# Performance work log

Measured on AMD Instinct MI355X. Metric: run time of the kernel, lower is better.

The kernel has to match this reference:

```python
import jax, jax.numpy as jnp
import numpy as np

BLUR = 0.05
P = 2
EPS_FINAL = BLUR ** P          # geomloss: eps = blur**p = 0.0025
DIAMETER = 2.0                 # max cosine cost magnitude
SCALING = 0.5                  # geomloss default; eps decays by scaling**p per step
N_FINAL_ITERS = 4              # extra balancing iterations at the final eps


def eps_schedule():
    eps_list = []
    e = DIAMETER ** P
    while e > EPS_FINAL:
        eps_list.append(e)
        e = e * (SCALING ** P)
    eps_list.extend([EPS_FINAL] * N_FINAL_ITERS)
    return eps_list


def cosine_cost(a, b):
    # a: (N, D), b: (M, D) -> (N, M) cost = 1 - cos_sim
    an = a / (jnp.linalg.norm(a, axis=1, keepdims=True) + 1e-12)
    bn = b / (jnp.linalg.norm(b, axis=1, keepdims=True) + 1e-12)
    return 1.0 - an @ bn.T


def softmin(C, pot, log_w, eps):
    # -eps * LSE_j( log_w + (pot_j - C_ij)/eps ) ; C: (N, M), pot: (M,)
    return -eps * jax.nn.logsumexp(log_w + (pot[None, :] - C) / eps, axis=1)


def sinkhorn_divergence(Cxy, Cxx, Cyy):
    N, M = Cxy.shape
    log_a = -jnp.log(jnp.asarray(N, dtype=Cxy.dtype))  # uniform weights
    log_b = -jnp.log(jnp.asarray(M, dtype=Cxy.dtype))
    sg = jax.lax.stop_gradient
    # Sinkhorn iterations run on detached costs (geomloss envelope-theorem trick)
    Cxy_s, Cxx_s, Cyy_s = sg(Cxy), sg(Cxx), sg(Cyy)
    f = jnp.zeros((N,), Cxy.dtype)
    g = jnp.zeros((M,), Cxy.dtype)
    fxx = jnp.zeros((N,), Cxy.dtype)
    gyy = jnp.zeros((M,), Cxy.dtype)
    for eps in eps_schedule():
        # symmetric (debiasing) potentials: averaged fixed-point update
        fxx = 0.5 * (fxx + softmin(Cxx_s, fxx, log_a, eps))
        gyy = 0.5 * (gyy + softmin(Cyy_s, gyy, log_b, eps))
        # cross potentials: simultaneous (Jacobi) update
        f, g = softmin(Cxy_s, g, log_b, eps), softmin(Cxy_s.T, f, log_a, eps)
    # final extrapolation step with gradients flowing through the costs
    eps = EPS_FINAL
    f_fin = softmin(Cxy, sg(g), log_b, eps)
    g_fin = softmin(Cxy.T, sg(f), log_a, eps)
    fxx_fin = softmin(Cxx, sg(fxx), log_a, eps)
    gyy_fin = softmin(Cyy, sg(gyy), log_b, eps)
    return jnp.mean(f_fin - fxx_fin) + jnp.mean(g_fin - gyy_fin)


def setup_inputs() -> dict:
    key = jax.random.key(0)
    k1, k2, k3 = jax.random.split(key, 3)
    x1 = jax.random.normal(k1, (8192, 256), dtype=jnp.float32)
    x2 = jax.random.normal(k2, (8192, 256), dtype=jnp.float32)
    w = jax.random.uniform(k3, (256,), dtype=jnp.float32)
    return {"x1": x1, "x2": x2, "w": w}


def reference(x1, x2, w):
    # Dist_loss.forward: clamp+renormalize learned per-feature weights, scale x1
    w_c = jnp.clip(w, 0.0, 2.0)
    w_c = w_c / jnp.mean(w_c)
    a = w_c[None, :] * x1
    Cxy = cosine_cost(a, x2)
    Cxx = cosine_cost(a, a)
    Cyy = cosine_cost(x2, x2)
    return sinkhorn_divergence(Cxy, Cxx, Cyy)
```

## Files before the change

kernel.cpp:

```cpp
#include <hip/hip_runtime.h>
#include <math.h>

#define N 8192
#define D 256
#define LN2 0.6931471805599453f
#define LDSROW 280
#define TSLOTS 1152

typedef short short8 __attribute__((ext_vector_type(8)));
typedef float f32x16 __attribute__((ext_vector_type(16)));
typedef unsigned short ushort;

__device__ __forceinline__ float fexp2(float x) { return __builtin_amdgcn_exp2f(x); }
__device__ __forceinline__ float flog2(float x) { return __builtin_amdgcn_logf(x); }

__device__ __forceinline__ ushort bf16r(float x) {
    unsigned int u = __float_as_uint(x);
    return (ushort)((u + 0x7FFF + ((u >> 16) & 1)) >> 16);
}

__device__ __forceinline__ void gl_lds16(const ushort* g, ushort* l) {
    __builtin_amdgcn_global_load_lds(
        (const __attribute__((address_space(1))) unsigned int*)g,
        (__attribute__((address_space(3))) unsigned int*)l, 16, 0, 0);
}

__global__ void prep_wc(const float* __restrict__ w, float* __restrict__ wc) {
    int t = threadIdx.x;
    float v = fminf(fmaxf(w[t], 0.0f), 2.0f);
    float s = v;
#pragma unroll
    for (int m = 1; m < 64; m <<= 1) s += __shfl_xor(s, m);
    __shared__ float sm[4];
    if ((t & 63) == 0) sm[t >> 6] = s;
    __syncthreads();
    float mean = (sm[0] + sm[1] + sm[2] + sm[3]) * (1.0f / 256.0f);
    wc[t] = v / mean;
}

__global__ void prep_normalize(const float* __restrict__ x1, const float* __restrict__ x2,
                               const float* __restrict__ wc,
                               ushort* __restrict__ an_i, ushort* __restrict__ bn_i) {
    int row = blockIdx.x;
    int t = threadIdx.x;
    int r; float v; ushort* ip;
    if (row < N) { r = row;     v = x1[(size_t)r * D + t] * wc[t]; ip = an_i; }
    else         { r = row - N; v = x2[(size_t)r * D + t];         ip = bn_i; }
    float ss = v * v;
#pragma unroll
    for (int m = 1; m < 64; m <<= 1) ss += __shfl_xor(ss, m);
    __shared__ float sm[4];
    if ((t & 63) == 0) sm[t >> 6] = ss;
    __syncthreads();
    float denom = sqrtf(sm[0] + sm[1] + sm[2] + sm[3]) + 1e-12f;
    ip[(size_t)r * D + t] = bf16r(v / denom);
}

__global__ void init_pots(float* __restrict__ pots, float* __restrict__ potm1) {
    int id = blockIdx.x * 256 + threadIdx.x;
    pots[id] = 0.0f;
    potm1[id] = -1.0f;
}

__global__ __launch_bounds__(256, 2) void softmin_mfma(
    const ushort* __restrict__ an_i, const ushort* __restrict__ bn_i,
    const float* __restrict__ potm1,
    float2* __restrict__ parts, float k1) {
    int bx = blockIdx.x;
    int k = bx & 7;
    int q = bx >> 3;
    int task = k >> 1;
    int split = ((k & 1) << 1) | (q & 1);
    int rb = q >> 1;
    const ushort* jp = (task == 0 || task == 3) ? an_i : bn_i;
    const ushort* ip = (task == 0 || task == 2) ? an_i : bn_i;
    const float* pm1 = potm1 + (size_t)task * N;

    int t = threadIdx.x;
    int wave = t >> 6, lane = t & 63;
    int l31 = lane & 31, lh = lane >> 5;
    int i0 = rb * 256 + wave * 64;

    __shared__ ushort lbuf[2][TSLOTS * 8];

    short8 bi0[16], bi1[16];
    {
        const ushort* ib = ip + (size_t)(i0 + l31) * D + lh * 8;
#pragma unroll
        for (int c = 0; c < 16; ++c) {
            bi0[c] = *(const short8*)(ib + c * 16);
            bi1[c] = *(const short8*)(ib + (size_t)32 * D + c * 16);
        }
    }
#pragma unroll
    for (int c = 0; c < 16; ++c) {
        asm volatile("" : "+a"(bi0[c]), "+a"(bi1[c]));
    }

    const int jbase0 = split * 2048;

    auto stage = [&](int b, int js) {
        const ushort* gb = jp + (size_t)(jbase0 + js * 32) * D;
        ushort* lb = &lbuf[b][0];
#pragma unroll
        for (int r = 0; r < 5; ++r) {
            if (r == 4 && t >= 128) break;
            int s = r * 256 + t;
            int row = s / 35;
            int c = s - row * 35;
            row = row > 31 ? 31 : row;
            c = c > 31 ? 31 : c;
            gl_lds16(gb + row * D + c * 8, lb + s * 8);
        }
    };

    float m0 = -INFINITY, s0 = 0.0f, m1 = -INFINITY, s1 = 0.0f;

    stage(0, 0);
    for (int js = 0; js < 64; ++js) {
        int cur = js & 1;
        __syncthreads();

        int j0 = jbase0 + js * 32;
        float pjk[16];
#pragma unroll
        for (int g = 0; g < 4; ++g) {
            float4 pv = *(const float4*)&pm1[j0 + 8 * g + 4 * lh];
            pjk[4 * g + 0] = pv.x * k1; pjk[4 * g + 1] = pv.y * k1;
            pjk[4 * g + 2] = pv.z * k1; pjk[4 * g + 3] = pv.w * k1;
        }

        if (js < 63) stage(cur ^ 1, js + 1);

        const ushort* lrow = &lbuf[cur][l31 * LDSROW + lh * 8];
        f32x16 acc0 = {}; f32x16 acc1 = {};
#pragma unroll
        for (int c = 0; c < 16; ++c) {
            short8 af = *(const short8*)(lrow + c * 16);
            acc0 = __builtin_amdgcn_mfma_f32_32x32x16_bf16(af, bi0[c], acc0, 0, 0, 0);
            acc1 = __builtin_amdgcn_mfma_f32_32x32x16_bf16(af, bi1[c], acc1, 0, 0, 0);
        }

        {
            float tv[16];
#pragma unroll
            for (int r = 0; r < 16; ++r) tv[r] = fmaf(acc0[r], k1, pjk[r]);
            float tm = tv[0];
#pragma unroll
            for (int r = 1; r < 16; ++r) tm = fmaxf(tm, tv[r]);
            float mn = fmaxf(m0, tm);
            float ad = 0.0f;
#pragma unroll
            for (int r = 0; r < 16; ++r) ad += fexp2(tv[r] - mn);
            s0 = s0 * fexp2(m0 - mn) + ad; m0 = mn;
        }
        {
            float tv[16];
#pragma unroll
            for (int r = 0; r < 16; ++r) tv[r] = fmaf(acc1[r], k1, pjk[r]);
            float tm = tv[0];
#pragma unroll
            for (int r = 1; r < 16; ++r) tm = fmaxf(tm, tv[r]);
            float mn = fmaxf(m1, tm);
            float ad = 0.0f;
#pragma unroll
            for (int r = 0; r < 16; ++r) ad += fexp2(tv[r] - mn);
            s1 = s1 * fexp2(m1 - mn) + ad; m1 = mn;
        }
    }
    float mo = __shfl_xor(m0, 32), so = __shfl_xor(s0, 32);
    float M0 = fmaxf(m0, mo);
    float S0 = s0 * fexp2(m0 - M0) + so * fexp2(mo - M0);
    mo = __shfl_xor(m1, 32); so = __shfl_xor(s1, 32);
    float M1 = fmaxf(m1, mo);
    float S1 = s1 * fexp2(m1 - M1) + so * fexp2(mo - M1);
    if (lane < 32) {
        size_t r0 = (size_t)task * N + (i0 + l31);
        size_t r1 = r0 + 32;
        parts[r0 * 4 + split] = make_float2(M0, S0);
        parts[r1 * 4 + split] = make_float2(M1, S1);
    }
}

__global__ void merge_pots(const float2* __restrict__ parts, float* __restrict__ pots,
                           float* __restrict__ potm1, float eps, float logw, int do_avg) {
    int id = blockIdx.x * 256 + threadIdx.x;
    int task = id >> 13;
    int row = id & (N - 1);
    const float2* p = parts + (size_t)id * 4;
    float2 a = p[0], b = p[1], c = p[2], d = p[3];
    float M = fmaxf(fmaxf(a.x, b.x), fmaxf(c.x, d.x));
    float S = a.y * fexp2(a.x - M) + b.y * fexp2(b.x - M) +
              c.y * fexp2(c.x - M) + d.y * fexp2(d.x - M);
    float lse = LN2 * (M + flog2(S));
    float v = -eps * (logw + lse);
    if (do_avg && task < 2) v = 0.5f * (pots[id] + v);
    pots[id] = v;
    int ct = (task < 2) ? task : (5 - task);
    potm1[(size_t)ct * N + row] = v - 1.0f;
}

__global__ void final_reduce(const float* __restrict__ pots, float* __restrict__ out) {
    int t = threadIdx.x;
    float s = 0.0f;
    for (int i = t; i < N; i += 256)
        s += (pots[2 * N + i] - pots[i]) + (pots[3 * N + i] - pots[N + i]);
#pragma unroll
    for (int m = 1; m < 64; m <<= 1) s += __shfl_xor(s, m);
    __shared__ float sm[4];
    if ((t & 63) == 0) sm[t >> 6] = s;
    __syncthreads();
    if (t == 0) out[0] = (sm[0] + sm[1] + sm[2] + sm[3]) * (1.0f / (float)N);
}

extern "C" void kernel_launch(void* const* d_in, const int* in_sizes, int n_in,
                              void* d_out, int out_size, void* d_ws, size_t ws_size,
                              hipStream_t stream) {
    const float* x1 = (const float*)d_in[0];
    const float* x2 = (const float*)d_in[1];
    const float* w  = (const float*)d_in[2];
    float* out = (float*)d_out;

    ushort* an_i = (ushort*)d_ws;
    ushort* bn_i = an_i + (size_t)N * D;
    float*  wc   = (float*)(bn_i + (size_t)N * D);
    float*  pots = wc + 256;
    float*  potm1 = pots + 4 * N;
    float2* parts = (float2*)(potm1 + 4 * N);

    prep_wc<<<1, 256, 0, stream>>>(w, wc);
    prep_normalize<<<2 * N, 256, 0, stream>>>(x1, x2, wc, an_i, bn_i);
    init_pots<<<4 * N / 256, 256, 0, stream>>>(pots, potm1);

    const float eps_list[10] = {4.0f, 1.0f, 0.25f, 0.0625f, 0.015625f,
                                0.00390625f, 0.0025f, 0.0025f, 0.0025f, 0.0025f};
    const float logw = -logf((float)N);
    const float LOG2E = 1.4426950408889634f;
    for (int it = 0; it < 10; ++it) {
        softmin_mfma<<<512, 256, 0, stream>>>(an_i, bn_i, potm1, parts, LOG2E / eps_list[it]);
        merge_pots<<<4 * N / 256, 256, 0, stream>>>(parts, pots, potm1,
                                                    eps_list[it], logw, 1);
    }
    softmin_mfma<<<512, 256, 0, stream>>>(an_i, bn_i, potm1, parts, LOG2E / 0.0025f);
    merge_pots<<<4 * N / 256, 256, 0, stream>>>(parts, pots, potm1, 0.0025f, logw, 0);
    final_reduce<<<1, 256, 0, stream>>>(pots, out);
}
```

Baseline: 1.813 ms.

## Repartition softmin into 768 blocks with 32 rows per wave and 3-way column split

Each wave now owns one 32-row tile instead of two, and the column range is split three ways (86/86/84 tiles) instead of four, so the grid becomes 768 blocks at three blocks per CU. The merge kernel combines three partial logsumexp pairs per row. The aim is a more even spread of work across CUs and higher occupancy through fewer registers per thread. The cost is that each LDS-staged column tile now feeds only one MFMA chain per wave instead of two, halving reuse of the shared tile and raising LDS and global traffic per FLOP.

```diff
diff --git a/kernel.cpp b/kernel.cpp
--- a/kernel.cpp
+++ b/kernel.cpp
@@ -62,16 +62,15 @@
     potm1[id] = -1.0f;
 }
 
-__global__ __launch_bounds__(256, 2) void softmin_mfma(
+__global__ __launch_bounds__(256, 3) void softmin_mfma(
     const ushort* __restrict__ an_i, const ushort* __restrict__ bn_i,
     const float* __restrict__ potm1,
     float2* __restrict__ parts, float k1) {
     int bx = blockIdx.x;
-    int k = bx & 7;
-    int q = bx >> 3;
-    int task = k >> 1;
-    int split = ((k & 1) << 1) | (q & 1);
-    int rb = q >> 1;
+    int c = bx % 12;
+    int rb = bx / 12;
+    int task = c & 3;
+    int split = c >> 2;
     const ushort* jp = (task == 0 || task == 3) ? an_i : bn_i;
     const ushort* ip = (task == 0 || task == 2) ? an_i : bn_i;
     const float* pm1 = potm1 + (size_t)task * N;
@@ -79,49 +78,48 @@
     int t = threadIdx.x;
     int wave = t >> 6, lane = t & 63;
     int l31 = lane & 31, lh = lane >> 5;
-    int i0 = rb * 256 + wave * 64;
+    int i0 = rb * 128 + wave * 32;
 
     __shared__ ushort lbuf[2][TSLOTS * 8];
 
-    short8 bi0[16], bi1[16];
+    short8 bi[16];
     {
         const ushort* ib = ip + (size_t)(i0 + l31) * D + lh * 8;
 #pragma unroll
-        for (int c = 0; c < 16; ++c) {
-            bi0[c] = *(const short8*)(ib + c * 16);
-            bi1[c] = *(const short8*)(ib + (size_t)32 * D + c * 16);
-        }
-    }
-#pragma unroll
-    for (int c = 0; c < 16; ++c) {
-        asm volatile("" : "+a"(bi0[c]), "+a"(bi1[c]));
-    }
-
-    const int jbase0 = split * 2048;
+        for (int cc = 0; cc < 16; ++cc) bi[cc] = *(const short8*)(ib + cc * 16);
+    }
+#pragma unroll
+    for (int cc = 0; cc < 16; ++cc) {
+        asm volatile("" : "+a"(bi[cc]));
+    }
+
+    int jb = split * 86;
+    int je = (split == 2) ? 256 : jb + 86;
 
     auto stage = [&](int b, int js) {
-        const ushort* gb = jp + (size_t)(jbase0 + js * 32) * D;
+        const ushort* gb = jp + (size_t)js * 32 * D;
         ushort* lb = &lbuf[b][0];
 #pragma unroll
         for (int r = 0; r < 5; ++r) {
             if (r == 4 && t >= 128) break;
             int s = r * 256 + t;
             int row = s / 35;
-            int c = s - row * 35;
+            int cs = s - row * 35;
             row = row > 31 ? 31 : row;
-            c = c > 31 ? 31 : c;
-            gl_lds16(gb + row * D + c * 8, lb + s * 8);
+            cs = cs > 31 ? 31 : cs;
+            gl_lds16(gb + row * D + cs * 8, lb + s * 8);
         }
     };
 
-    float m0 = -INFINITY, s0 = 0.0f, m1 = -INFINITY, s1 = 0.0f;
-
-    stage(0, 0);
-    for (int js = 0; js < 64; ++js) {
+    float m0 = -INFINITY, s0 = 0.0f;
+
+    stage(0, jb);
+    for (int js = jb; js < je; ++js) {
         int cur = js & 1;
         __syncthreads();
-
-        int j0 = jbase0 + js * 32;
+        if (js + 1 < je) stage(cur ^ 1, js + 1);
+
+        int j0 = js * 32;
         float pjk[16];
 #pragma unroll
         for (int g = 0; g < 4; ++g) {
@@ -130,55 +128,32 @@
             pjk[4 * g + 2] = pv.z * k1; pjk[4 * g + 3] = pv.w * k1;
         }
 
-        if (js < 63) stage(cur ^ 1, js + 1);
-
         const ushort* lrow = &lbuf[cur][l31 * LDSROW + lh * 8];
-        f32x16 acc0 = {}; f32x16 acc1 = {};
-#pragma unroll
-        for (int c = 0; c < 16; ++c) {
-            short8 af = *(const short8*)(lrow + c * 16);
-            acc0 = __builtin_amdgcn_mfma_f32_32x32x16_bf16(af, bi0[c], acc0, 0, 0, 0);
-            acc1 = __builtin_amdgcn_mfma_f32_32x32x16_bf16(af, bi1[c], acc1, 0, 0, 0);
+        f32x16 acc = {};
+#pragma unroll
+        for (int cc = 0; cc < 16; ++cc) {
+            short8 af = *(const short8*)(lrow + cc * 16);
+            acc = __builtin_amdgcn_mfma_f32_32x32x16_bf16(af, bi[cc], acc, 0, 0, 0);
         }
 
-        {
-            float tv[16];
-#pragma unroll
-            for (int r = 0; r < 16; ++r) tv[r] = fmaf(acc0[r], k1, pjk[r]);
-            float tm = tv[0];
-#pragma unroll
-            for (int r = 1; r < 16; ++r) tm = fmaxf(tm, tv[r]);
-            float mn = fmaxf(m0, tm);
-            float ad = 0.0f;
-#pragma unroll
-            for (int r = 0; r < 16; ++r) ad += fexp2(tv[r] - mn);
-            s0 = s0 * fexp2(m0 - mn) + ad; m0 = mn;
-        }
-        {
-            float tv[16];
-#pragma unroll
-            for (int r = 0; r < 16; ++r) tv[r] = fmaf(acc1[r], k1, pjk[r]);
-            float tm = tv[0];
-#pragma unroll
-            for (int r = 1; r < 16; ++r) tm = fmaxf(tm, tv[r]);
-            float mn = fmaxf(m1, tm);
-            float ad = 0.0f;
-#pragma unroll
-            for (int r = 0; r < 16; ++r) ad += fexp2(tv[r] - mn);
-            s1 = s1 * fexp2(m1 - mn) + ad; m1 = mn;
-        }
+        float tv[16];
+#pragma unroll
+        for (int r = 0; r < 16; ++r) tv[r] = fmaf(acc[r], k1, pjk[r]);
+        float tm = tv[0];
+#pragma unroll
+        for (int r = 1; r < 16; ++r) tm = fmaxf(tm, tv[r]);
+        float mn = fmaxf(m0, tm);
+        float ad = 0.0f;
+#pragma unroll
+        for (int r = 0; r < 16; ++r) ad += fexp2(tv[r] - mn);
+        s0 = s0 * fexp2(m0 - mn) + ad; m0 = mn;
     }
     float mo = __shfl_xor(m0, 32), so = __shfl_xor(s0, 32);
     float M0 = fmaxf(m0, mo);
     float S0 = s0 * fexp2(m0 - M0) + so * fexp2(mo - M0);
-    mo = __shfl_xor(m1, 32); so = __shfl_xor(s1, 32);
-    float M1 = fmaxf(m1, mo);
-    float S1 = s1 * fexp2(m1 - M1) + so * fexp2(mo - M1);
     if (lane < 32) {
         size_t r0 = (size_t)task * N + (i0 + l31);
-        size_t r1 = r0 + 32;
-        parts[r0 * 4 + split] = make_float2(M0, S0);
-        parts[r1 * 4 + split] = make_float2(M1, S1);
+        parts[r0 * 3 + split] = make_float2(M0, S0);
     }
 }
 
@@ -187,11 +162,10 @@
     int id = blockIdx.x * 256 + threadIdx.x;
     int task = id >> 13;
     int row = id & (N - 1);
-    const float2* p = parts + (size_t)id * 4;
-    float2 a = p[0], b = p[1], c = p[2], d = p[3];
-    float M = fmaxf(fmaxf(a.x, b.x), fmaxf(c.x, d.x));
-    float S = a.y * fexp2(a.x - M) + b.y * fexp2(b.x - M) +
-              c.y * fexp2(c.x - M) + d.y * fexp2(d.x - M);
+    const float2* p = parts + (size_t)id * 3;
+    float2 a = p[0], b = p[1], c = p[2];
+    float M = fmaxf(fmaxf(a.x, b.x), c.x);
+    float S = a.y * fexp2(a.x - M) + b.y * fexp2(b.x - M) + c.y * fexp2(c.x - M);
     float lse = LN2 * (M + flog2(S));
     float v = -eps * (logw + lse);
     if (do_avg && task < 2) v = 0.5f * (pots[id] + v);
@@ -237,11 +211,11 @@
     const float logw = -logf((float)N);
     const float LOG2E = 1.4426950408889634f;
     for (int it = 0; it < 10; ++it) {
-        softmin_mfma<<<512, 256, 0, stream>>>(an_i, bn_i, potm1, parts, LOG2E / eps_list[it]);
+        softmin_mfma<<<768, 256, 0, stream>>>(an_i, bn_i, potm1, parts, LOG2E / eps_list[it]);
         merge_pots<<<4 * N / 256, 256, 0, stream>>>(parts, pots, potm1,
                                                     eps_list[it], logw, 1);
     }
-    softmin_mfma<<<512, 256, 0, stream>>>(an_i, bn_i, potm1, parts, LOG2E / 0.0025f);
+    softmin_mfma<<<768, 256, 0, stream>>>(an_i, bn_i, potm1, parts, LOG2E / 0.0025f);
     merge_pots<<<4 * N / 256, 256, 0, stream>>>(parts, pots, potm1, 0.0025f, logw, 0);
     final_reduce<<<1, 256, 0, stream>>>(pots, out);
 }
```

Result: no change. 1.847 ms (+1.8%).
